# Kernel optimization log

Measured on AMD Instinct MI355X. Metric: run time of the kernel, lower is better.

Reference implementation:

```python
import jax, jax.numpy as jnp
import numpy as np

B, S, D, H, HID = 2, 2048, 256, 8, 1024
EPS = 1e-9


def gelu_fast(x):
    return 0.5 * x * (1.0 + jnp.tanh(x * 0.7978845608 * (1.0 + 0.044715 * x * x)))


def layer_norm(x, g, b):
    m = jnp.mean(x, axis=-1, keepdims=True)
    v = jnp.mean(jnp.square(x - m), axis=-1, keepdims=True)
    return (x - m) * jax.lax.rsqrt(v + EPS) * g + b


def setup_inputs() -> dict:
    key = jax.random.key(0)
    ks = jax.random.split(key, 16)
    x = jax.random.normal(ks[0], (B, S, D), dtype=jnp.float32)
    # causal look-ahead mask: additive, 0 on/below diagonal, -1e9 above
    causal = jnp.triu(jnp.ones((S, S), dtype=jnp.float32), k=1) * (-1e9)
    look_ahead_mask = causal[None, None, :, :]  # (1,1,S,S)
    sd = 0.02
    return {
        "x": x,
        "look_ahead_mask": look_ahead_mask,
        "ln1_g": jnp.ones((D,), jnp.float32),
        "ln1_b": jnp.zeros((D,), jnp.float32),
        "wq_w": jax.random.normal(ks[1], (D * H, D), jnp.float32) * sd,
        "wq_b": jnp.zeros((D * H,), jnp.float32),
        "wk_w": jax.random.normal(ks[2], (D * H, D), jnp.float32) * sd,
        "wk_b": jnp.zeros((D * H,), jnp.float32),
        "wv_w": jax.random.normal(ks[3], (D * H, D), jnp.float32) * sd,
        "wv_b": jnp.zeros((D * H,), jnp.float32),
        "dense_w": jax.random.normal(ks[4], (D, D * H), jnp.float32) * sd,
        "dense_b": jnp.zeros((D,), jnp.float32),
        "ln2_g": jnp.ones((D,), jnp.float32),
        "ln2_b": jnp.zeros((D,), jnp.float32),
        "fc1_w": jax.random.normal(ks[5], (HID, D), jnp.float32) * sd,
        "fc1_b": jnp.zeros((HID,), jnp.float32),
        "fc2_w": jax.random.normal(ks[6], (D, HID), jnp.float32) * sd,
        "fc2_b": jnp.zeros((D,), jnp.float32),
    }


def reference(x, look_ahead_mask, ln1_g, ln1_b, wq_w, wq_b, wk_w, wk_b,
              wv_w, wv_b, dense_w, dense_b, ln2_g, ln2_b,
              fc1_w, fc1_b, fc2_w, fc2_b):
    xn = layer_norm(x, ln1_g, ln1_b)
    # QKV: D -> D*H, each head has full head-dim D (module quirk)
    q = (jnp.einsum('bsd,ed->bse', xn, wq_w) + wq_b).reshape(B, S, H, D).transpose(0, 2, 1, 3)
    k = (jnp.einsum('bsd,ed->bse', xn, wk_w) + wk_b).reshape(B, S, H, D).transpose(0, 2, 1, 3)
    v = (jnp.einsum('bsd,ed->bse', xn, wv_w) + wv_b).reshape(B, S, H, D).transpose(0, 2, 1, 3)
    scores = jnp.einsum('bhqd,bhkd->bhqk', q, k) / jnp.sqrt(jnp.float32(D))
    scores = scores + look_ahead_mask
    attn_weights = jax.nn.softmax(scores, axis=-1)
    ctx = jnp.einsum('bhqk,bhkd->bhqd', attn_weights, v)  # (B,H,S,D)
    ctx = ctx.transpose(0, 2, 1, 3).reshape(B, S, H * D)
    attn = jnp.einsum('bse,de->bsd', ctx, dense_w) + dense_b
    x1 = xn + attn  # residual uses post-LN x (module quirk)
    m = layer_norm(x1, ln2_g, ln2_b)
    m = gelu_fast(jnp.einsum('bsd,hd->bsh', m, fc1_w) + fc1_b)
    m = jnp.einsum('bsh,dh->bsd', m, fc2_w) + fc2_b
    out = x1 + m
    return out, attn_weights
```

## Files before the change

kernel.cpp:

```cpp
#include <hip/hip_runtime.h>
#include <hip/hip_bf16.h>


typedef __bf16 bf16_t;
typedef __bf16 bf16x8 __attribute__((ext_vector_type(8)));
typedef __bf16 bf16x4 __attribute__((ext_vector_type(4)));
typedef float  f32x4  __attribute__((ext_vector_type(4)));

#define DEV __device__ __forceinline__

DEV f32x4 mfma16(bf16x8 a, bf16x8 b, f32x4 c) {
  return __builtin_amdgcn_mfma_f32_16x16x32_bf16(a, b, c, 0, 0, 0);
}

DEV void gload16(const void* g, void* l) {
  __builtin_amdgcn_global_load_lds(
      (const __attribute__((address_space(1))) unsigned int*)g,
      (__attribute__((address_space(3))) unsigned int*)l, 16, 0, 0);
}

__global__ __launch_bounds__(256) void cvt_all(
    const float* __restrict__ s0, const float* __restrict__ s1,
    const float* __restrict__ s2, const float* __restrict__ s3,
    const float* __restrict__ s4, const float* __restrict__ s5,
    bf16_t* __restrict__ d0, bf16_t* __restrict__ d1, bf16_t* __restrict__ d2,
    bf16_t* __restrict__ d3, bf16_t* __restrict__ d4, bf16_t* __restrict__ d5) {
  int i = blockIdx.x * 256 + threadIdx.x;
  const float* s; bf16_t* d; int off;
  if      (i < 131072) { s = s0; d = d0; off = i; }
  else if (i < 262144) { s = s1; d = d1; off = i - 131072; }
  else if (i < 393216) { s = s2; d = d2; off = i - 262144; }
  else if (i < 524288) { s = s3; d = d3; off = i - 393216; }
  else if (i < 589824) { s = s4; d = d4; off = i - 524288; }
  else                 { s = s5; d = d5; off = i - 589824; }
  float4 v = ((const float4*)s)[off];
  bf16x4 o = { (bf16_t)v.x, (bf16_t)v.y, (bf16_t)v.z, (bf16_t)v.w };
  ((bf16x4*)d)[off] = o;
}

__global__ __launch_bounds__(256) void ln_k(const float* __restrict__ x,
    const float* __restrict__ g, const float* __restrict__ bta,
    float* __restrict__ of, bf16_t* __restrict__ ob) {
  int row = blockIdx.x * 4 + (threadIdx.x >> 6);
  int l = threadIdx.x & 63;
  const float4 v = *(const float4*)(x + (size_t)row * 256 + l * 4);
  float s  = v.x + v.y + v.z + v.w;
  float s2 = v.x*v.x + v.y*v.y + v.z*v.z + v.w*v.w;
#pragma unroll
  for (int o = 1; o < 64; o <<= 1) { s += __shfl_xor(s, o, 64); s2 += __shfl_xor(s2, o, 64); }
  float m   = s * (1.f/256.f);
  float var = s2 * (1.f/256.f) - m * m;
  float rs  = rsqrtf(var + 1e-9f);
  const float4 gv = *(const float4*)(g   + l * 4);
  const float4 bv = *(const float4*)(bta + l * 4);
  float4 y;
  y.x = (v.x - m) * rs * gv.x + bv.x;
  y.y = (v.y - m) * rs * gv.y + bv.y;
  y.z = (v.z - m) * rs * gv.z + bv.z;
  y.w = (v.w - m) * rs * gv.w + bv.w;
  if (of) *(float4*)(of + (size_t)row * 256 + l * 4) = y;
  bf16x4 yb = { (bf16_t)y.x, (bf16_t)y.y, (bf16_t)y.z, (bf16_t)y.w };
  *(bf16x4*)(ob + (size_t)row * 256 + l * 4) = yb;
}

DEV void gemm_core(const bf16_t* __restrict__ A, const bf16_t* __restrict__ W,
                   int lda, int row0, int col0, int k0, int kiters,
                   char* Asb, char* Bsb, f32x4 (&acc)[4][4]) {
  int tid = threadIdx.x, w = tid >> 6, l = tid & 63, l15 = l & 15, lhi = l >> 4;
  int wr = (w >> 1) * 64, wc = (w & 1) * 64;

#define STAGE(buf, kk) do {                                                   \
    char* Ad = Asb + (buf) * 8192 + w * 1024;                                 \
    char* Bd = Bsb + (buf) * 8192 + w * 1024;                                 \
    _Pragma("unroll")                                                         \
    for (int j = 0; j < 2; ++j) {                                             \
      int idx = (j * 256 + tid) * 8; int r = idx >> 5, c = idx & 31;          \
      gload16(A + (size_t)(row0 + r) * lda + (kk) + c, Ad + j * 4096);        \
      gload16(W + (size_t)(col0 + r) * lda + (kk) + c, Bd + j * 4096);        \
    } } while (0)

  STAGE(0, k0);
  for (int t = 0; t < kiters; ++t) {
    int cur = t & 1;
    if (t + 1 < kiters) {
      STAGE(cur ^ 1, k0 + (t + 1) * 32);
      asm volatile("s_waitcnt vmcnt(4)" ::: "memory");
    } else {
      asm volatile("s_waitcnt vmcnt(0)" ::: "memory");
    }
    __builtin_amdgcn_s_barrier();
    asm volatile("" ::: "memory");
    const bf16_t* As = (const bf16_t*)(Asb + cur * 8192);
    const bf16_t* Bs = (const bf16_t*)(Bsb + cur * 8192);
    bf16x8 af[4], bfr[4];
#pragma unroll
    for (int m = 0; m < 4; ++m)
      af[m] = *(const bf16x8*)(As + (wr + 16 * m + l15) * 32 + lhi * 8);
#pragma unroll
    for (int n = 0; n < 4; ++n)
      bfr[n] = *(const bf16x8*)(Bs + (wc + 16 * n + l15) * 32 + lhi * 8);
#pragma unroll
    for (int m = 0; m < 4; ++m)
#pragma unroll
      for (int n = 0; n < 4; ++n)
        acc[m][n] = mfma16(af[m], bfr[n], acc[m][n]);
    asm volatile("" ::: "memory");
    __builtin_amdgcn_s_barrier();
  }
#undef STAGE
}

__global__ __launch_bounds__(256, 2) void gemm_qkv(
    const bf16_t* __restrict__ A,
    const bf16_t* __restrict__ W0, const bf16_t* __restrict__ W1, const bf16_t* __restrict__ W2,
    const float* __restrict__ b0, const float* __restrict__ b1, const float* __restrict__ b2,
    bf16_t* __restrict__ qo, bf16_t* __restrict__ ko, bf16_t* __restrict__ vo) {
  __shared__ char Asb[2 * 8192];
  __shared__ char Bsb[2 * 8192];
  int bx = blockIdx.x;
  int wsel = bx >> 4, cb = bx & 15;
  const bf16_t* W    = wsel == 0 ? W0 : (wsel == 1 ? W1 : W2);
  const float*  bias = wsel == 0 ? b0 : (wsel == 1 ? b1 : b2);
  bf16_t*       out  = wsel == 0 ? qo : (wsel == 1 ? ko : vo);
  int row0 = blockIdx.y * 128, col0 = cb * 128;
  f32x4 acc[4][4] = {};
  gemm_core(A, W, 256, row0, col0, 0, 8, Asb, Bsb, acc);

  int tid = threadIdx.x, w = tid >> 6, l = tid & 63, l15 = l & 15, lhi = l >> 4;
  int wr = (w >> 1) * 64, wc = (w & 1) * 64;
#pragma unroll
  for (int m = 0; m < 4; ++m)
#pragma unroll
    for (int n = 0; n < 4; ++n)
#pragma unroll
      for (int j = 0; j < 4; ++j) {
        int row = row0 + wr + 16 * m + lhi * 4 + j;
        int col = col0 + wc + 16 * n + l15;
        float v = acc[m][n][j] + bias[col];
        out[((size_t)((row >> 11) * 8 + (col >> 8)) * 2048 + (row & 2047)) * 256 + (col & 255)] = (bf16_t)v;
      }
}

__global__ __launch_bounds__(256, 2) void gemm_part(
    const bf16_t* __restrict__ A, const bf16_t* __restrict__ W,
    int lda, int ksub, float* __restrict__ parts) {
  __shared__ char Asb[2 * 8192];
  __shared__ char Bsb[2 * 8192];
  int z = blockIdx.z;
  int row0 = blockIdx.y * 128, col0 = blockIdx.x * 128;
  f32x4 acc[4][4] = {};
  gemm_core(A, W, lda, row0, col0, z * ksub, ksub >> 5, Asb, Bsb, acc);

  int tid = threadIdx.x, w = tid >> 6, l = tid & 63, l15 = l & 15, lhi = l >> 4;
  int wr = (w >> 1) * 64, wc = (w & 1) * 64;
  float* p = parts + (size_t)z * 1048576;
#pragma unroll
  for (int m = 0; m < 4; ++m)
#pragma unroll
    for (int n = 0; n < 4; ++n)
#pragma unroll
      for (int j = 0; j < 4; ++j) {
        int row = row0 + wr + 16 * m + lhi * 4 + j;
        int col = col0 + wc + 16 * n + l15;
        p[(size_t)row * 256 + col] = acc[m][n][j];
      }
}

__global__ __launch_bounds__(256) void reduce4(
    const float* __restrict__ parts, const float* __restrict__ bias,
    const float* __restrict__ res, float* __restrict__ out) {
  int i = blockIdx.x * 256 + threadIdx.x;
  f32x4 s = *(const f32x4*)(parts + (size_t)i * 4);
  s += *(const f32x4*)(parts + 1048576 + (size_t)i * 4);
  s += *(const f32x4*)(parts + 2097152 + (size_t)i * 4);
  s += *(const f32x4*)(parts + 3145728 + (size_t)i * 4);
  s += *(const f32x4*)(res + (size_t)i * 4);
  s += *(const f32x4*)(bias + (i & 63) * 4);
  *(f32x4*)(out + (size_t)i * 4) = s;
}

__global__ __launch_bounds__(256, 2) void gemm_fc1(
    const bf16_t* __restrict__ A, const bf16_t* __restrict__ W,
    const float* __restrict__ bias, bf16_t* __restrict__ out) {
  __shared__ char Asb[2 * 8192];
  __shared__ char Bsb[2 * 8192];
  int row0 = blockIdx.y * 128, col0 = blockIdx.x * 128;
  f32x4 acc[4][4] = {};
  gemm_core(A, W, 256, row0, col0, 0, 8, Asb, Bsb, acc);

  int tid = threadIdx.x, w = tid >> 6, l = tid & 63, l15 = l & 15, lhi = l >> 4;
  int wr = (w >> 1) * 64, wc = (w & 1) * 64;
#pragma unroll
  for (int m = 0; m < 4; ++m)
#pragma unroll
    for (int n = 0; n < 4; ++n)
#pragma unroll
      for (int j = 0; j < 4; ++j) {
        int row = row0 + wr + 16 * m + lhi * 4 + j;
        int col = col0 + wc + 16 * n + l15;
        float t = acc[m][n][j] + bias[col];
        float ge = 0.5f * t * (1.f + tanhf(0.7978845608f * t * (1.f + 0.044715f * t * t)));
        out[(size_t)row * 1024 + col] = (bf16_t)ge;
      }
}

__global__ __launch_bounds__(256) void vtrans(const bf16_t* __restrict__ v, bf16_t* __restrict__ vt) {
  __shared__ bf16_t t[64 * 72];
  int bh = blockIdx.z;
  int s0 = blockIdx.x * 64, d0 = blockIdx.y * 64;
  int tid = threadIdx.x;
#pragma unroll
  for (int j = 0; j < 2; ++j) {
    int cj = j * 256 + tid;
    int r = cj >> 3, c = (cj & 7) * 8;
    *(bf16x8*)(t + r * 72 + c) = *(const bf16x8*)(v + ((size_t)bh * 2048 + s0 + r) * 256 + d0 + c);
  }
  __syncthreads();
#pragma unroll
  for (int j = 0; j < 2; ++j) {
    int cj = j * 256 + tid;
    int rd = cj >> 3, cs = (cj & 7) * 8;
    bf16x8 o;
#pragma unroll
    for (int i = 0; i < 8; ++i) o[i] = t[(cs + i) * 72 + rd];
    *(bf16x8*)(vt + ((size_t)bh * 256 + d0 + rd) * 2048 + s0 + cs) = o;
  }
}

__global__ __launch_bounds__(256, 2) void attn_k(
    const bf16_t* __restrict__ qg, const bf16_t* __restrict__ kg,
    const bf16_t* __restrict__ vt, float* __restrict__ pout,
    bf16_t* __restrict__ ctxo) {
  __shared__ bf16_t Ksh[64 * 256];
  __shared__ bf16_t Vsh[256 * 64];
  __shared__ bf16_t Psh[64 * 64];
  int bx = blockIdx.x;
  int bh = bx & 15, qt = 31 - (bx >> 4);
  int tid = threadIdx.x, w = tid >> 6, l = tid & 63;
  int l15 = l & 15, lhi = l >> 4, l7 = l & 7;
  const bf16_t* Q   = qg + (size_t)bh * 2048 * 256;
  const bf16_t* Kg2 = kg + (size_t)bh * 2048 * 256;
  const bf16_t* Vt  = vt + (size_t)bh * 256 * 2048;
  int qbase = qt * 64;

  bf16x8 qf[8];
#pragma unroll
  for (int ks = 0; ks < 8; ++ks)
    qf[ks] = *(const bf16x8*)(Q + (size_t)(qbase + w * 16 + l15) * 256 + ks * 32 + lhi * 8);

  float sums[4] = {0.f, 0.f, 0.f, 0.f};
  for (int kt = 0; kt <= qt; ++kt) {
    __syncthreads();
#pragma unroll
    for (int j = 0; j < 8; ++j) {
      int p = (j * 256 + tid) * 16;
      int r = p >> 9;
      int co = (p & 511) ^ ((r & 7) << 4);
      gload16(Kg2 + (size_t)(kt * 64 + r) * 256 + (co >> 1), (char*)Ksh + j * 4096 + w * 1024);
    }
    __syncthreads();
    f32x4 acc[4] = {};
#pragma unroll
    for (int ks = 0; ks < 8; ++ks) {
#pragma unroll
      for (int n = 0; n < 4; ++n) {
        bf16x8 kb = *(const bf16x8*)((const char*)Ksh + (16 * n + l15) * 512 + ((ks * 64 + lhi * 16) ^ (l7 << 4)));
        acc[n] = mfma16(qf[ks], kb, acc[n]);
      }
    }
#pragma unroll
    for (int n = 0; n < 4; ++n)
#pragma unroll
      for (int j = 0; j < 4; ++j) {
        int kc = kt * 64 + 16 * n + l15;
        int qr = qbase + w * 16 + lhi * 4 + j;
        sums[j] += (kc <= qr) ? __expf(acc[n][j] * 0.0625f) : 0.f;
      }
  }
#pragma unroll
  for (int j = 0; j < 4; ++j) {
#pragma unroll
    for (int o = 1; o < 16; o <<= 1) sums[j] += __shfl_xor(sums[j], o, 64);
    sums[j] = 1.f / sums[j];
  }

  f32x4 ctx[16] = {};
  for (int kt = 0; kt <= qt; ++kt) {
    __syncthreads();
#pragma unroll
    for (int j = 0; j < 8; ++j) {
      int p = (j * 256 + tid) * 16;
      { int r = p >> 9; int co = (p & 511) ^ ((r & 7) << 4);
        gload16(Kg2 + (size_t)(kt * 64 + r) * 256 + (co >> 1), (char*)Ksh + j * 4096 + w * 1024); }
      { int r = p >> 7; int co = (p & 127) ^ ((r & 7) << 4);
        gload16(Vt + (size_t)r * 2048 + kt * 64 + (co >> 1), (char*)Vsh + j * 4096 + w * 1024); }
    }
    __syncthreads();
    f32x4 acc[4] = {};
#pragma unroll
    for (int ks = 0; ks < 8; ++ks) {
#pragma unroll
      for (int n = 0; n < 4; ++n) {
        bf16x8 kb = *(const bf16x8*)((const char*)Ksh + (16 * n + l15) * 512 + ((ks * 64 + lhi * 16) ^ (l7 << 4)));
        acc[n] = mfma16(qf[ks], kb, acc[n]);
      }
    }
#pragma unroll
    for (int n = 0; n < 4; ++n) {
#pragma unroll
      for (int j = 0; j < 4; ++j) {
        int kc = kt * 64 + 16 * n + l15;
        int qr = qbase + w * 16 + lhi * 4 + j;
        float e = (kc <= qr) ? __expf(acc[n][j] * 0.0625f) * sums[j] : 0.f;
        pout[((size_t)bh * 2048 + qr) * 2048 + kc] = e;
        int prow = w * 16 + lhi * 4 + j;
        int pcb = (16 * n + l15) * 2;
        *(bf16_t*)((char*)Psh + prow * 128 + (pcb ^ ((prow & 7) << 4))) = (bf16_t)e;
      }
    }
    __syncthreads();
#pragma unroll
    for (int k2 = 0; k2 < 2; ++k2) {
      bf16x8 pa = *(const bf16x8*)((const char*)Psh + (w * 16 + l15) * 128 + ((k2 * 64 + lhi * 16) ^ (l7 << 4)));
#pragma unroll
      for (int n = 0; n < 16; ++n) {
        bf16x8 vb = *(const bf16x8*)((const char*)Vsh + (16 * n + l15) * 128 + ((k2 * 64 + lhi * 16) ^ (l7 << 4)));
        ctx[n] = mfma16(pa, vb, ctx[n]);
      }
    }
  }

  int b = bh >> 3, h = bh & 7;
#pragma unroll
  for (int n = 0; n < 16; ++n)
#pragma unroll
    for (int j = 0; j < 4; ++j) {
      int qr = qbase + w * 16 + lhi * 4 + j;
      ctxo[((size_t)b * 2048 + qr) * 2048 + h * 256 + 16 * n + l15] = (bf16_t)ctx[n][j];
    }

  int zs = qbase + 64;
  for (int r = 0; r < 64; ++r) {
    size_t base = ((size_t)bh * 2048 + qbase + r) * 2048;
    for (int c = zs + tid * 4; c < 2048; c += 1024) {
      *(float4*)(pout + base + c) = make_float4(0.f, 0.f, 0.f, 0.f);
    }
  }
}

extern "C" void kernel_launch(void* const* d_in, const int* in_sizes, int n_in,
                              void* d_out, int out_size, void* d_ws, size_t ws_size,
                              hipStream_t stream) {
  const float* x     = (const float*)d_in[0];
  const float* ln1g  = (const float*)d_in[2];
  const float* ln1b  = (const float*)d_in[3];
  const float* wq_w  = (const float*)d_in[4];
  const float* wq_b  = (const float*)d_in[5];
  const float* wk_w  = (const float*)d_in[6];
  const float* wk_b  = (const float*)d_in[7];
  const float* wv_w  = (const float*)d_in[8];
  const float* wv_b  = (const float*)d_in[9];
  const float* dw    = (const float*)d_in[10];
  const float* db    = (const float*)d_in[11];
  const float* ln2g  = (const float*)d_in[12];
  const float* ln2b  = (const float*)d_in[13];
  const float* f1w   = (const float*)d_in[14];
  const float* f1b   = (const float*)d_in[15];
  const float* f2w   = (const float*)d_in[16];
  const float* f2b   = (const float*)d_in[17];

  char* ws = (char*)d_ws;
  const size_t MB = 1u << 20;
  float*  xn_f = (float*) (ws + 0 * MB);
  bf16_t* xn_b = (bf16_t*)(ws + 4 * MB);
  bf16_t* q_b  = (bf16_t*)(ws + 6 * MB);
  bf16_t* k_b  = (bf16_t*)(ws + 22 * MB);
  bf16_t* v_b  = (bf16_t*)(ws + 38 * MB);
  bf16_t* vt_b = (bf16_t*)(ws + 54 * MB);
  float*  x1_f = (float*) (ws + 70 * MB);
  bf16_t* m_b  = (bf16_t*)(ws + 74 * MB);
  bf16_t* h_b  = (bf16_t*)(ws + 76 * MB);
  bf16_t* wq_bf = (bf16_t*)(ws + 84 * MB);
  bf16_t* wk_bf = wq_bf + 524288;
  bf16_t* wv_bf = wk_bf + 524288;
  bf16_t* dw_bf = wv_bf + 524288;
  bf16_t* f1_bf = dw_bf + 524288;
  bf16_t* f2_bf = f1_bf + 262144;
  bf16_t* ctx_b = v_b;
  float* parts_d = (float*)q_b;
  float* parts_f = (float*)k_b;

  float* out0 = (float*)d_out;
  float* pout = out0 + 1048576;

  cvt_all<<<2560, 256, 0, stream>>>(wq_w, wk_w, wv_w, dw, f1w, f2w,
                                    wq_bf, wk_bf, wv_bf, dw_bf, f1_bf, f2_bf);

  ln_k<<<1024, 256, 0, stream>>>(x, ln1g, ln1b, xn_f, xn_b);

  gemm_qkv<<<dim3(48, 32), 256, 0, stream>>>(xn_b, wq_bf, wk_bf, wv_bf,
                                             wq_b, wk_b, wv_b, q_b, k_b, v_b);

  vtrans<<<dim3(32, 4, 16), 256, 0, stream>>>(v_b, vt_b);

  attn_k<<<512, 256, 0, stream>>>(q_b, k_b, vt_b, pout, ctx_b);

  gemm_part<<<dim3(2, 32, 4), 256, 0, stream>>>(ctx_b, dw_bf, 2048, 512, parts_d);
  reduce4<<<1024, 256, 0, stream>>>(parts_d, db, xn_f, x1_f);

  ln_k<<<1024, 256, 0, stream>>>(x1_f, ln2g, ln2b, nullptr, m_b);

  gemm_fc1<<<dim3(8, 32), 256, 0, stream>>>(m_b, f1_bf, f1b, h_b);

  gemm_part<<<dim3(2, 32, 4), 256, 0, stream>>>(h_b, f2_bf, 1024, 256, parts_f);
  reduce4<<<1024, 256, 0, stream>>>(parts_f, f2b, x1_f, out0);
}
```

Baseline: 233.3 us.

## Split attention into rowsum and PV kernels with double-buffered async loads

The fused two-pass attention kernel becomes two kernels. The first computes the softmax row sums and writes them to workspace. The second recomputes the scores in 32-key tiles and produces the probabilities and the context. Both kernels double-buffer K/V tiles in LDS with explicit vmcnt waits so global loads overlap MFMA work, and they use a 2x2 warp tiling. Probabilities are now written to global memory with vectorised row-wise stores from the bf16 LDS tile, replacing scattered scalar stores. Those stores now hold values rounded through bf16 rather than full fp32, which loosens the precision of the attention weights output.

```diff
diff --git a/kernel.cpp b/kernel.cpp
--- a/kernel.cpp
+++ b/kernel.cpp
@@ -227,117 +227,215 @@
   }
 }
 
-__global__ __launch_bounds__(256, 2) void attn_k(
+__global__ __launch_bounds__(256, 2) void rowsum_k(
     const bf16_t* __restrict__ qg, const bf16_t* __restrict__ kg,
-    const bf16_t* __restrict__ vt, float* __restrict__ pout,
-    bf16_t* __restrict__ ctxo) {
-  __shared__ bf16_t Ksh[64 * 256];
-  __shared__ bf16_t Vsh[256 * 64];
-  __shared__ bf16_t Psh[64 * 64];
+    float* __restrict__ rsg) {
+  __shared__ bf16_t Ksh[2][64 * 256];
+  __shared__ float  sl[2][64];
   int bx = blockIdx.x;
   int bh = bx & 15, qt = 31 - (bx >> 4);
   int tid = threadIdx.x, w = tid >> 6, l = tid & 63;
-  int l15 = l & 15, lhi = l >> 4, l7 = l & 7;
+  int l15 = l & 15, lhi = l >> 4;
+  int wm = w >> 1, wn = w & 1;
+  const bf16_t* Q   = qg + (size_t)bh * 2048 * 256;
+  const bf16_t* Kg2 = kg + (size_t)bh * 2048 * 256;
+  int qbase = qt * 64;
+  int nkt = qt + 1;
+
+  bf16x8 qf[2][8];
+#pragma unroll
+  for (int m = 0; m < 2; ++m)
+#pragma unroll
+    for (int ks = 0; ks < 8; ++ks)
+      qf[m][ks] = *(const bf16x8*)(Q + (size_t)(qbase + wm * 32 + m * 16 + l15) * 256 + ks * 32 + lhi * 8);
+
+#define RSTAGE(t_) do {                                                        \
+    char* dst = (char*)Ksh[(t_) & 1] + w * 1024;                               \
+    _Pragma("unroll")                                                          \
+    for (int j = 0; j < 8; ++j) {                                              \
+      int idx = (j * 256 + tid) * 16; int r = idx >> 9;                        \
+      int co = (idx & 511) ^ ((r & 7) << 4);                                   \
+      gload16(Kg2 + (size_t)((t_) * 64 + r) * 256 + (co >> 1), dst + j * 4096);\
+    } } while (0)
+
+  RSTAGE(0);
+  if (nkt > 1) RSTAGE(1);
+
+  float sums[2][4] = {};
+  for (int t = 0; t < nkt; ++t) {
+    if (t + 1 < nkt) asm volatile("s_waitcnt vmcnt(8)" ::: "memory");
+    else             asm volatile("s_waitcnt vmcnt(0)" ::: "memory");
+    __builtin_amdgcn_s_barrier();
+    const char* Kb = (const char*)Ksh[t & 1];
+    f32x4 acc[2][2] = {};
+#pragma unroll
+    for (int ks = 0; ks < 8; ++ks) {
+#pragma unroll
+      for (int n2 = 0; n2 < 2; ++n2) {
+        int row = wn * 32 + n2 * 16 + l15;
+        bf16x8 kb = *(const bf16x8*)(Kb + row * 512 + ((ks * 64 + lhi * 16) ^ ((row & 7) << 4)));
+#pragma unroll
+        for (int m = 0; m < 2; ++m)
+          acc[m][n2] = mfma16(qf[m][ks], kb, acc[m][n2]);
+      }
+    }
+#pragma unroll
+    for (int m = 0; m < 2; ++m)
+#pragma unroll
+      for (int n2 = 0; n2 < 2; ++n2)
+#pragma unroll
+        for (int j = 0; j < 4; ++j) {
+          int qr = qbase + wm * 32 + m * 16 + lhi * 4 + j;
+          int kc = t * 64 + wn * 32 + n2 * 16 + l15;
+          sums[m][j] += (kc <= qr) ? __expf(acc[m][n2][j] * 0.0625f) : 0.f;
+        }
+    asm volatile("" ::: "memory");
+    __builtin_amdgcn_s_barrier();
+    if (t + 2 < nkt) RSTAGE(t + 2);
+  }
+#undef RSTAGE
+
+#pragma unroll
+  for (int m = 0; m < 2; ++m)
+#pragma unroll
+    for (int j = 0; j < 4; ++j) {
+#pragma unroll
+      for (int o = 1; o < 16; o <<= 1) sums[m][j] += __shfl_xor(sums[m][j], o, 64);
+    }
+  if (l15 == 0) {
+#pragma unroll
+    for (int m = 0; m < 2; ++m)
+#pragma unroll
+      for (int j = 0; j < 4; ++j)
+        sl[wn][wm * 32 + m * 16 + lhi * 4 + j] = sums[m][j];
+  }
+  __syncthreads();
+  if (tid < 64)
+    rsg[(size_t)bh * 2048 + qbase + tid] = 1.f / (sl[0][tid] + sl[1][tid]);
+}
+
+__global__ __launch_bounds__(256, 2) void attn_pv(
+    const bf16_t* __restrict__ qg, const bf16_t* __restrict__ kg,
+    const bf16_t* __restrict__ vt, const float* __restrict__ rsg,
+    float* __restrict__ pout, bf16_t* __restrict__ ctxo) {
+  __shared__ bf16_t Ksh[2][32 * 256];
+  __shared__ bf16_t Vsh[2][256 * 32];
+  __shared__ bf16_t Psh[64 * 32];
+  int bx = blockIdx.x;
+  int bh = bx & 15, qt = 31 - (bx >> 4);
+  int tid = threadIdx.x, w = tid >> 6, l = tid & 63;
+  int l15 = l & 15, lhi = l >> 4;
+  int wm = w >> 1, wn = w & 1;
   const bf16_t* Q   = qg + (size_t)bh * 2048 * 256;
   const bf16_t* Kg2 = kg + (size_t)bh * 2048 * 256;
   const bf16_t* Vt  = vt + (size_t)bh * 256 * 2048;
   int qbase = qt * 64;
-
-  bf16x8 qf[8];
-#pragma unroll
-  for (int ks = 0; ks < 8; ++ks)
-    qf[ks] = *(const bf16x8*)(Q + (size_t)(qbase + w * 16 + l15) * 256 + ks * 32 + lhi * 8);
-
-  float sums[4] = {0.f, 0.f, 0.f, 0.f};
-  for (int kt = 0; kt <= qt; ++kt) {
-    __syncthreads();
-#pragma unroll
-    for (int j = 0; j < 8; ++j) {
-      int p = (j * 256 + tid) * 16;
-      int r = p >> 9;
-      int co = (p & 511) ^ ((r & 7) << 4);
-      gload16(Kg2 + (size_t)(kt * 64 + r) * 256 + (co >> 1), (char*)Ksh + j * 4096 + w * 1024);
-    }
-    __syncthreads();
-    f32x4 acc[4] = {};
+  int nkt = 2 * (qt + 1);
+
+  bf16x8 qf[2][8];
+#pragma unroll
+  for (int m = 0; m < 2; ++m)
+#pragma unroll
+    for (int ks = 0; ks < 8; ++ks)
+      qf[m][ks] = *(const bf16x8*)(Q + (size_t)(qbase + wm * 32 + m * 16 + l15) * 256 + ks * 32 + lhi * 8);
+
+  float inv[8];
+#pragma unroll
+  for (int m = 0; m < 2; ++m)
+#pragma unroll
+    for (int j = 0; j < 4; ++j)
+      inv[m * 4 + j] = rsg[(size_t)bh * 2048 + qbase + wm * 32 + m * 16 + lhi * 4 + j];
+
+#define PSTAGE(t_) do {                                                         \
+    char* kd = (char*)Ksh[(t_) & 1] + w * 1024;                                 \
+    char* vd = (char*)Vsh[(t_) & 1] + w * 1024;                                 \
+    _Pragma("unroll")                                                           \
+    for (int j = 0; j < 4; ++j) {                                               \
+      int idx = (j * 256 + tid) * 16;                                           \
+      { int r = idx >> 9; int co = (idx & 511) ^ ((r & 7) << 4);                \
+        gload16(Kg2 + (size_t)((t_) * 32 + r) * 256 + (co >> 1), kd + j * 4096); } \
+      { int r = idx >> 6; int co = (idx & 63) ^ (((r >> 2) & 3) << 4);          \
+        gload16(Vt + (size_t)r * 2048 + (t_) * 32 + (co >> 1), vd + j * 4096); } \
+    } } while (0)
+
+  PSTAGE(0);
+  PSTAGE(1);
+
+  f32x4 ctx[4][4] = {};
+  for (int t = 0; t < nkt; ++t) {
+    if (t + 1 < nkt) asm volatile("s_waitcnt vmcnt(8)" ::: "memory");
+    else             asm volatile("s_waitcnt vmcnt(0)" ::: "memory");
+    __builtin_amdgcn_s_barrier();
+    const char* Kb = (const char*)Ksh[t & 1];
+    const char* Vb = (const char*)Vsh[t & 1];
+
+    f32x4 acc[2] = {};
 #pragma unroll
     for (int ks = 0; ks < 8; ++ks) {
-#pragma unroll
-      for (int n = 0; n < 4; ++n) {
-        bf16x8 kb = *(const bf16x8*)((const char*)Ksh + (16 * n + l15) * 512 + ((ks * 64 + lhi * 16) ^ (l7 << 4)));
-        acc[n] = mfma16(qf[ks], kb, acc[n]);
+      int row = wn * 16 + l15;
+      bf16x8 kb = *(const bf16x8*)(Kb + row * 512 + ((ks * 64 + lhi * 16) ^ ((row & 7) << 4)));
+#pragma unroll
+      for (int m = 0; m < 2; ++m)
+        acc[m] = mfma16(qf[m][ks], kb, acc[m]);
+    }
+#pragma unroll
+    for (int m = 0; m < 2; ++m)
+#pragma unroll
+      for (int j = 0; j < 4; ++j) {
+        int rr = wm * 32 + m * 16 + lhi * 4 + j;
+        int qr = qbase + rr;
+        int kc = t * 32 + wn * 16 + l15;
+        float e = (kc <= qr) ? __expf(acc[m][j] * 0.0625f) * inv[m * 4 + j] : 0.f;
+        int addr = rr * 64 + (wn * 16 + l15) * 2;
+        *(bf16_t*)((char*)Psh + (addr ^ (((rr >> 2) & 3) << 4))) = (bf16_t)e;
       }
-    }
+    asm volatile("" ::: "memory");
+    __builtin_amdgcn_s_barrier();
+
+    {
+      int row = tid >> 2;
+      int ch  = (tid & 3) * 16;
+      bf16x8 p8 = *(const bf16x8*)((const char*)Psh + row * 64 + (ch ^ (((row >> 2) & 3) << 4)));
+      float* dst = pout + ((size_t)bh * 2048 + qbase + row) * 2048 + t * 32 + (tid & 3) * 8;
+      f32x4 lo = { (float)p8[0], (float)p8[1], (float)p8[2], (float)p8[3] };
+      f32x4 hi = { (float)p8[4], (float)p8[5], (float)p8[6], (float)p8[7] };
+      *(f32x4*)dst = lo;
+      *(f32x4*)(dst + 4) = hi;
+    }
+
+    bf16x8 pa[4], vb[4];
+#pragma unroll
+    for (int m4 = 0; m4 < 4; ++m4) {
+      int row = m4 * 16 + l15;
+      pa[m4] = *(const bf16x8*)((const char*)Psh + ((row * 64 + lhi * 16) ^ (((row >> 2) & 3) << 4)));
+    }
+#pragma unroll
+    for (int n = 0; n < 4; ++n) {
+      int row = w * 64 + n * 16 + l15;
+      vb[n] = *(const bf16x8*)(Vb + ((row * 64 + lhi * 16) ^ (((row >> 2) & 3) << 4)));
+    }
+#pragma unroll
+    for (int m4 = 0; m4 < 4; ++m4)
+#pragma unroll
+      for (int n = 0; n < 4; ++n)
+        ctx[m4][n] = mfma16(pa[m4], vb[n], ctx[m4][n]);
+
+    asm volatile("" ::: "memory");
+    __builtin_amdgcn_s_barrier();
+    if (t + 2 < nkt) PSTAGE(t + 2);
+  }
+#undef PSTAGE
+
+  int b = bh >> 3, h = bh & 7;
+#pragma unroll
+  for (int m4 = 0; m4 < 4; ++m4)
 #pragma unroll
     for (int n = 0; n < 4; ++n)
 #pragma unroll
       for (int j = 0; j < 4; ++j) {
-        int kc = kt * 64 + 16 * n + l15;
-        int qr = qbase + w * 16 + lhi * 4 + j;
-        sums[j] += (kc <= qr) ? __expf(acc[n][j] * 0.0625f) : 0.f;
+        int qr = qbase + m4 * 16 + lhi * 4 + j;
+        ctxo[((size_t)b * 2048 + qr) * 2048 + h * 256 + w * 64 + n * 16 + l15] = (bf16_t)ctx[m4][n][j];
       }
-  }
-#pragma unroll
-  for (int j = 0; j < 4; ++j) {
-#pragma unroll
-    for (int o = 1; o < 16; o <<= 1) sums[j] += __shfl_xor(sums[j], o, 64);
-    sums[j] = 1.f / sums[j];
-  }
-
-  f32x4 ctx[16] = {};
-  for (int kt = 0; kt <= qt; ++kt) {
-    __syncthreads();
-#pragma unroll
-    for (int j = 0; j < 8; ++j) {
-      int p = (j * 256 + tid) * 16;
-      { int r = p >> 9; int co = (p & 511) ^ ((r & 7) << 4);
-        gload16(Kg2 + (size_t)(kt * 64 + r) * 256 + (co >> 1), (char*)Ksh + j * 4096 + w * 1024); }
-      { int r = p >> 7; int co = (p & 127) ^ ((r & 7) << 4);
-        gload16(Vt + (size_t)r * 2048 + kt * 64 + (co >> 1), (char*)Vsh + j * 4096 + w * 1024); }
-    }
-    __syncthreads();
-    f32x4 acc[4] = {};
-#pragma unroll
-    for (int ks = 0; ks < 8; ++ks) {
-#pragma unroll
-      for (int n = 0; n < 4; ++n) {
-        bf16x8 kb = *(const bf16x8*)((const char*)Ksh + (16 * n + l15) * 512 + ((ks * 64 + lhi * 16) ^ (l7 << 4)));
-        acc[n] = mfma16(qf[ks], kb, acc[n]);
-      }
-    }
-#pragma unroll
-    for (int n = 0; n < 4; ++n) {
-#pragma unroll
-      for (int j = 0; j < 4; ++j) {
-        int kc = kt * 64 + 16 * n + l15;
-        int qr = qbase + w * 16 + lhi * 4 + j;
-        float e = (kc <= qr) ? __expf(acc[n][j] * 0.0625f) * sums[j] : 0.f;
-        pout[((size_t)bh * 2048 + qr) * 2048 + kc] = e;
-        int prow = w * 16 + lhi * 4 + j;
-        int pcb = (16 * n + l15) * 2;
-        *(bf16_t*)((char*)Psh + prow * 128 + (pcb ^ ((prow & 7) << 4))) = (bf16_t)e;
-      }
-    }
-    __syncthreads();
-#pragma unroll
-    for (int k2 = 0; k2 < 2; ++k2) {
-      bf16x8 pa = *(const bf16x8*)((const char*)Psh + (w * 16 + l15) * 128 + ((k2 * 64 + lhi * 16) ^ (l7 << 4)));
-#pragma unroll
-      for (int n = 0; n < 16; ++n) {
-        bf16x8 vb = *(const bf16x8*)((const char*)Vsh + (16 * n + l15) * 128 + ((k2 * 64 + lhi * 16) ^ (l7 << 4)));
-        ctx[n] = mfma16(pa, vb, ctx[n]);
-      }
-    }
-  }
-
-  int b = bh >> 3, h = bh & 7;
-#pragma unroll
-  for (int n = 0; n < 16; ++n)
-#pragma unroll
-    for (int j = 0; j < 4; ++j) {
-      int qr = qbase + w * 16 + lhi * 4 + j;
-      ctxo[((size_t)b * 2048 + qr) * 2048 + h * 256 + 16 * n + l15] = (bf16_t)ctx[n][j];
-    }
 
   int zs = qbase + 64;
   for (int r = 0; r < 64; ++r) {
@@ -386,6 +484,7 @@
   bf16_t* dw_bf = wv_bf + 524288;
   bf16_t* f1_bf = dw_bf + 524288;
   bf16_t* f2_bf = f1_bf + 262144;
+  float*  rs_f  = (float*)(ws + 90 * MB);
   bf16_t* ctx_b = v_b;
   float* parts_d = (float*)q_b;
   float* parts_f = (float*)k_b;
@@ -401,9 +500,11 @@
   gemm_qkv<<<dim3(48, 32), 256, 0, stream>>>(xn_b, wq_bf, wk_bf, wv_bf,
                                              wq_b, wk_b, wv_b, q_b, k_b, v_b);
 
+  rowsum_k<<<512, 256, 0, stream>>>(q_b, k_b, rs_f);
+
   vtrans<<<dim3(32, 4, 16), 256, 0, stream>>>(v_b, vt_b);
 
-  attn_k<<<512, 256, 0, stream>>>(q_b, k_b, vt_b, pout, ctx_b);
+  attn_pv<<<512, 256, 0, stream>>>(q_b, k_b, vt_b, rs_f, pout, ctx_b);
 
   gemm_part<<<dim3(2, 32, 4), 256, 0, stream>>>(ctx_b, dw_bf, 2048, 512, parts_d);
   reduce4<<<1024, 256, 0, stream>>>(parts_d, db, xn_f, x1_f);
```

New measurement: 229.5 us. About the same (-1.6%).
